# Optimization experiments

Hardware: AMD Instinct MI355X
Metric: run time of the kernel (lower is better)

## Reference

```python
import jax, jax.numpy as jnp
import numpy as np

B, S, H, T, NF = 64, 512, 1024, 4, 12
P = NF * (NF - 1) // 2  # 66 step pairs


def _head(x, w1, b1, w2, b2):
    # LinearsHead (eval mode: dropout = identity): linear -> relu -> linear
    return jax.nn.relu(x @ w1 + b1) @ w2 + b2


def setup_inputs() -> dict:
    key = jax.random.key(0)
    ks = jax.random.split(key, 12)
    sc = 0.02
    # non-overlapping contiguous spans: targets then facts, each L tokens
    L = S // (T + NF)  # 32
    t_start = jnp.arange(T, dtype=jnp.int32) * L
    f_start = (T + jnp.arange(NF, dtype=jnp.int32)) * L
    target_offsets = jnp.broadcast_to(jnp.stack([t_start, t_start + L], -1), (B, T, 2))
    fact_offsets = jnp.broadcast_to(jnp.stack([f_start, f_start + L], -1), (B, NF, 2))
    return {
        'seq_features': jax.random.normal(ks[0], (B, S, H), jnp.float32),
        'cls_features': jax.random.normal(ks[1], (B, H), jnp.float32),
        'target_offsets': target_offsets,
        'fact_offsets': fact_offsets,
        'fact_score_mask': jnp.ones((B, NF, T), jnp.float32),
        'sentsim_w1': sc * jax.random.normal(ks[2], (2 * H, H), jnp.float32),
        'sentsim_b1': jnp.zeros((H,), jnp.float32),
        'sentsim_w2': sc * jax.random.normal(ks[3], (H, 1), jnp.float32),
        'sentsim_b2': jnp.zeros((1,), jnp.float32),
        'step_w1': sc * jax.random.normal(ks[4], (2 * H, H), jnp.float32),
        'step_b1': jnp.zeros((H,), jnp.float32),
        'step_w2': sc * jax.random.normal(ks[5], (H, 1), jnp.float32),
        'step_b2': jnp.zeros((1,), jnp.float32),
        'state_w1': sc * jax.random.normal(ks[6], (H, H), jnp.float32),
        'state_b1': jnp.zeros((H,), jnp.float32),
        'state_w2': sc * jax.random.normal(ks[7], (H, 1), jnp.float32),
        'state_b2': jnp.zeros((1,), jnp.float32),
        'abd_w1': sc * jax.random.normal(ks[8], (2 * H, H), jnp.float32),
        'abd_b1': jnp.zeros((H,), jnp.float32),
        'abd_w2': sc * jax.random.normal(ks[9], (H, 1), jnp.float32),
        'abd_b2': jnp.zeros((1,), jnp.float32),
        'lambda_weight': jnp.array([0.5, 0.5], jnp.float32),
    }


def reference(seq_features, cls_features, target_offsets, fact_offsets, fact_score_mask,
              sentsim_w1, sentsim_b1, sentsim_w2, sentsim_b2,
              step_w1, step_b1, step_w2, step_b2,
              state_w1, state_b1, state_w2, state_b2,
              abd_w1, abd_b1, abd_w2, abd_b2, lambda_weight):
    b, s, h = seq_features.shape
    t = target_offsets.shape[1]
    nf = fact_offsets.shape[1]
    pos = jnp.arange(s)

    def seg_mean(offs):  # offs [b,k,2] -> mean-pooled [b,k,h]
        m = ((pos >= offs[..., 0:1]) & (pos < offs[..., 1:2])).astype(seq_features.dtype)
        cnt = (offs[..., 1] - offs[..., 0]).astype(seq_features.dtype)[..., None]
        return jnp.einsum('bks,bsh->bkh', m, seq_features) / cnt

    tgt = seg_mean(target_offsets)  # [b,t,h]
    fct = seg_mean(fact_offsets)    # [b,nf,h]

    # fact-cls pairs ordered target-major: features[ti*nf+fi] = cat(fact, target)
    ff = jnp.broadcast_to(fct[:, None], (b, t, nf, h))
    tt = jnp.broadcast_to(tgt[:, :, None], (b, t, nf, h))
    pair = jnp.concatenate([ff, tt], -1).reshape(b, t * nf, 2 * h)
    fact_score = jax.nn.sigmoid(_head(pair, sentsim_w1, sentsim_b1, sentsim_w2, sentsim_b2)[..., 0])  # [b, t*nf]
    # original does .view(len(facts), len(targets)) on the flat t-major scores
    mat = fact_score.reshape(b, nf, t)
    max_per_fact = jnp.max(mat * fact_score_mask, axis=2)  # [b, nf]
    state_fact = jnp.mean(max_per_fact, axis=1)            # [b]
    state_cls = jax.nn.sigmoid(_head(cls_features, state_w1, state_b1, state_w2, state_b2)[..., 0])
    w = jax.nn.softmax(lambda_weight)
    state = w[0] * state_fact + w[1] * state_cls           # [b]

    # step pairs: combinations(range(nf), 2) == row-major triu indices
    i1, i2 = jnp.triu_indices(nf, k=1)
    step_feat = jnp.concatenate([fct[:, i1], fct[:, i2]], -1)  # [b,P,2h]
    step = _head(step_feat, step_w1, step_b1, step_w2, step_b2)[..., 0]  # [b,P]

    tside = jnp.mean(tgt, axis=1)  # sum/len over targets [b,h]
    abd_feat = jnp.concatenate([jnp.broadcast_to(tside[:, None], (b, nf, h)), fct], -1)
    abd = _head(abd_feat, abd_w1, abd_b1, abd_w2, abd_b2)[..., 0]  # [b,nf]

    # step_func == 'softmax_all': joint softmax over step + abd scores
    allsc = jax.nn.softmax(jnp.concatenate([step, abd], axis=1), axis=1)
    np_pairs = i1.shape[0]
    step, abd = allsc[:, :np_pairs], allsc[:, np_pairs:]

    # pack: [state | fact_score | step | step_abd]
    return jnp.concatenate([state[:, None], fact_score, step, abd], axis=1)
```

## Files before the change

### kernel.cpp

```cpp
#include <hip/hip_runtime.h>
#include <hip/hip_bf16.h>

#define B_    64
#define S_    512
#define H_    1024
#define HH_   (H_*H_)
#define T_    4
#define NF_   12
#define TNF_  48
#define NP_   66
#define OUTC_ 127

#define NSENT_ (B_*TNF_)
#define NSTEP_ (B_*NP_)
#define NABD_  (B_*NF_)
#define NCLS_  (B_)
#define NWAVES_ (NSENT_+NSTEP_+NABD_+NCLS_)

#define AROW_FCT   0
#define AROW_TGT   768
#define AROW_TSD   1024
#define AROW_CLS   1088
#define AROWS_     1152

#define GROW_FSENT 0
#define GROW_S1    768
#define GROW_S2    1536
#define GROW_AF    2304
#define GROW_TSENT 3072
#define GROW_AT    3328
#define GROW_CLS   3392
#define GROWS_     3456

typedef __bf16 bf16x8 __attribute__((ext_vector_type(8)));
typedef float  f32x4  __attribute__((ext_vector_type(4)));
typedef __attribute__((address_space(1))) const unsigned int gcu32;
typedef __attribute__((address_space(3))) unsigned int lu32;

__device__ __forceinline__ ushort f2bf(float x) {
    union { float f; unsigned u; } c; c.f = x;
    unsigned r = c.u + 0x7fffu + ((c.u >> 16) & 1u);
    return (ushort)(r >> 16);
}
__device__ __forceinline__ float bflo(unsigned u) {
    union { unsigned u; float f; } c; c.u = u << 16; return c.f;
}
__device__ __forceinline__ float bfhi(unsigned u) {
    union { unsigned u; float f; } c; c.u = u & 0xffff0000u; return c.f;
}

__global__ __launch_bounds__(256) void prep_kernel(
    const float* __restrict__ seq, const int* __restrict__ toffs,
    const int* __restrict__ foffs, const float* __restrict__ cls,
    const float* __restrict__ sw1, const float* __restrict__ pw1,
    const float* __restrict__ aw1, const float* __restrict__ cw1,
    float* __restrict__ tgt32, ushort* __restrict__ Abf,
    ushort* __restrict__ Wt)
{
    int blk = blockIdx.x;
    int tid = threadIdx.x;

    if (blk < 1024) {
        int b = blk >> 4;
        int k = blk & 15;
        int start, end, arow;
        float* dst32 = nullptr;
        if (k < T_) {
            start = toffs[(b*T_ + k)*2];
            end   = toffs[(b*T_ + k)*2 + 1];
            dst32 = tgt32 + (size_t)(b*T_ + k) * H_;
            arow  = AROW_TGT + b*T_ + k;
        } else {
            int f = k - T_;
            start = foffs[(b*NF_ + f)*2];
            end   = foffs[(b*NF_ + f)*2 + 1];
            arow  = AROW_FCT + b*NF_ + f;
        }
        int h0 = tid * 4;
        const float* base = seq + ((size_t)b * S_ + start) * H_ + h0;
        float4 s = make_float4(0.f, 0.f, 0.f, 0.f);
        int n = end - start;
        #pragma unroll 4
        for (int r = 0; r < n; ++r) {
            float4 v = *(const float4*)(base + (size_t)r * H_);
            s.x += v.x; s.y += v.y; s.z += v.z; s.w += v.w;
        }
        float inv = 1.f / (float)n;
        s.x *= inv; s.y *= inv; s.z *= inv; s.w *= inv;
        if (dst32) *(float4*)(dst32 + h0) = s;
        ushort4 q; q.x = f2bf(s.x); q.y = f2bf(s.y); q.z = f2bf(s.z); q.w = f2bf(s.w);
        *(ushort4*)(Abf + (size_t)arow * H_ + h0) = q;
    } else if (blk < 1088) {
        int b = blk - 1024;
        int h0 = tid * 4;
        float4 c = *(const float4*)(cls + (size_t)b * H_ + h0);
        ushort4 qc; qc.x = f2bf(c.x); qc.y = f2bf(c.y); qc.z = f2bf(c.z); qc.w = f2bf(c.w);
        *(ushort4*)(Abf + (size_t)(AROW_CLS + b) * H_ + h0) = qc;
    } else {
        __shared__ float Tt[32][33];
        int idx2 = blk - 1088;
        int z = idx2 >> 10;
        int rem = idx2 & 1023;
        int k0 = (rem >> 5) * 32;
        int n0 = (rem & 31) * 32;
        const float* src;
        switch (z) {
            case 0: src = sw1; break;
            case 1: src = pw1; break;
            case 2: src = pw1 + HH_; break;
            case 3: src = aw1 + HH_; break;
            case 4: src = sw1 + HH_; break;
            case 5: src = aw1; break;
            default: src = cw1; break;
        }
        int ty = tid >> 3, tx = tid & 7;
        float4 v = *(const float4*)(src + (size_t)(k0 + ty) * H_ + n0 + tx*4);
        Tt[ty][tx*4 + 0] = v.x; Tt[ty][tx*4 + 1] = v.y;
        Tt[ty][tx*4 + 2] = v.z; Tt[ty][tx*4 + 3] = v.w;
        __syncthreads();
        int nx = ty, kx = tx;
        ushort4 q;
        q.x = f2bf(Tt[kx*4 + 0][nx]); q.y = f2bf(Tt[kx*4 + 1][nx]);
        q.z = f2bf(Tt[kx*4 + 2][nx]); q.w = f2bf(Tt[kx*4 + 3][nx]);
        *(ushort4*)(Wt + (size_t)z * HH_ + (size_t)(n0 + nx) * H_ + k0 + kx*4) = q;
    }
}

__global__ __launch_bounds__(256) void tside_kernel(
    const float* __restrict__ tgt32, ushort* __restrict__ Abf)
{
    int b = blockIdx.x;
    int h0 = threadIdx.x * 4;
    float4 s = make_float4(0.f, 0.f, 0.f, 0.f);
    for (int t = 0; t < T_; ++t) {
        float4 v = *(const float4*)(tgt32 + (size_t)(b*T_ + t)*H_ + h0);
        s.x += v.x; s.y += v.y; s.z += v.z; s.w += v.w;
    }
    ushort4 q;
    q.x = f2bf(s.x*0.25f); q.y = f2bf(s.y*0.25f);
    q.z = f2bf(s.z*0.25f); q.w = f2bf(s.w*0.25f);
    *(ushort4*)(Abf + (size_t)(AROW_TSD + b) * H_ + h0) = q;
}

__global__ __launch_bounds__(256) void gemm_bf16_kernel(
    const ushort* __restrict__ Abf, const ushort* __restrict__ Wt,
    ushort* __restrict__ G)
{
    __shared__ __align__(16) ushort As[2][64*32];
    __shared__ __align__(16) ushort Bs[2][128*32];

    int bx = blockIdx.x;
    int arow_base, wsel, grow_base, mt;
    if (bx < 48)      { int j = bx / 12; mt = bx % 12; arow_base = AROW_FCT; wsel = j; grow_base = j * 768; }
    else if (bx < 52) { mt = bx - 48; arow_base = AROW_TGT; wsel = 4; grow_base = GROW_TSENT; }
    else if (bx == 52){ mt = 0; arow_base = AROW_TSD; wsel = 5; grow_base = GROW_AT; }
    else              { mt = 0; arow_base = AROW_CLS; wsel = 6; grow_base = GROW_CLS; }

    const int tid  = threadIdx.x;
    const int lane = tid & 63;
    const int w    = tid >> 6;
    const int wr   = w >> 1, wc = w & 1;
    const int m0   = mt * 64;
    const int n0   = blockIdx.y * 128;

    const int srow  = lane >> 2;
    const int scol8 = (lane & 3) * 8;
    const ushort* gA  = Abf + (size_t)(arow_base + m0 + w*16 + srow) * H_ + scol8;
    const ushort* gB0 = Wt + (size_t)wsel * HH_ + (size_t)(n0 + w*32 + srow) * H_ + scol8;
    const ushort* gB1 = gB0 + (size_t)16 * H_;

    f32x4 acc00 = {0,0,0,0}, acc01 = {0,0,0,0}, acc02 = {0,0,0,0}, acc03 = {0,0,0,0};
    f32x4 acc10 = {0,0,0,0}, acc11 = {0,0,0,0}, acc12 = {0,0,0,0}, acc13 = {0,0,0,0};

    const int frow = lane & 15;
    const int fk   = (lane >> 4) * 8;

    #define STAGE(buf, kk) do {                                                   \
        __builtin_amdgcn_global_load_lds((gcu32*)(gA  + (kk)), (lu32*)(As[buf] + w*512), 16, 0, 0);          \
        __builtin_amdgcn_global_load_lds((gcu32*)(gB0 + (kk)), (lu32*)(Bs[buf] + w*1024), 16, 0, 0);         \
        __builtin_amdgcn_global_load_lds((gcu32*)(gB1 + (kk)), (lu32*)(Bs[buf] + w*1024 + 512), 16, 0, 0);   \
    } while (0)

    STAGE(0, 0);
    __syncthreads();

    #pragma unroll 1
    for (int t = 0; t < 32; ++t) {
        const int cur = t & 1;
        if (t < 31) STAGE(cur ^ 1, (t + 1) * 32);

        const ushort* pa = As[cur] + (wr*32 + frow) * 32 + fk;
        const ushort* pb = Bs[cur] + (wc*64 + frow) * 32 + fk;
        bf16x8 a0 = *(const bf16x8*)pa;
        bf16x8 a1 = *(const bf16x8*)(pa + 512);
        bf16x8 b0 = *(const bf16x8*)pb;
        bf16x8 b1 = *(const bf16x8*)(pb + 512);
        bf16x8 b2 = *(const bf16x8*)(pb + 1024);
        bf16x8 b3 = *(const bf16x8*)(pb + 1536);

        acc00 = __builtin_amdgcn_mfma_f32_16x16x32_bf16(a0, b0, acc00, 0, 0, 0);
        acc01 = __builtin_amdgcn_mfma_f32_16x16x32_bf16(a0, b1, acc01, 0, 0, 0);
        acc02 = __builtin_amdgcn_mfma_f32_16x16x32_bf16(a0, b2, acc02, 0, 0, 0);
        acc03 = __builtin_amdgcn_mfma_f32_16x16x32_bf16(a0, b3, acc03, 0, 0, 0);
        acc10 = __builtin_amdgcn_mfma_f32_16x16x32_bf16(a1, b0, acc10, 0, 0, 0);
        acc11 = __builtin_amdgcn_mfma_f32_16x16x32_bf16(a1, b1, acc11, 0, 0, 0);
        acc12 = __builtin_amdgcn_mfma_f32_16x16x32_bf16(a1, b2, acc12, 0, 0, 0);
        acc13 = __builtin_amdgcn_mfma_f32_16x16x32_bf16(a1, b3, acc13, 0, 0, 0);

        if (t < 31) __syncthreads();
    }
    #undef STAGE

    const int r0 = (lane >> 4) * 4;
    const int c  = lane & 15;
    const size_t rowb = (size_t)(grow_base + m0 + wr*32);
    const size_t colb = (size_t)(n0 + wc*64);
    #pragma unroll
    for (int r = 0; r < 4; ++r) {
        size_t ra = (rowb + r0 + r) * H_ + colb;
        size_t rb = (rowb + 16 + r0 + r) * H_ + colb;
        G[ra + 0  + c] = f2bf(acc00[r]);
        G[ra + 16 + c] = f2bf(acc01[r]);
        G[ra + 32 + c] = f2bf(acc02[r]);
        G[ra + 48 + c] = f2bf(acc03[r]);
        G[rb + 0  + c] = f2bf(acc10[r]);
        G[rb + 16 + c] = f2bf(acc11[r]);
        G[rb + 32 + c] = f2bf(acc12[r]);
        G[rb + 48 + c] = f2bf(acc13[r]);
    }
}

__global__ __launch_bounds__(256) void combine_kernel(
    const ushort* __restrict__ G,
    const float* __restrict__ sb1, const float* __restrict__ sw2,
    const float* __restrict__ pb1, const float* __restrict__ pw2,
    const float* __restrict__ ab1, const float* __restrict__ aw2,
    const float* __restrict__ cb1, const float* __restrict__ cw2,
    float* __restrict__ ssent, float* __restrict__ sstep,
    float* __restrict__ sabd, float* __restrict__ scls)
{
    int wv = blockIdx.x * 4 + (threadIdx.x >> 6);
    int lane = threadIdx.x & 63;
    if (wv >= NWAVES_) return;

    const ushort *U, *V;
    const float *b1, *w2;
    float* outp;
    if (wv < NSENT_) {
        int b = wv / TNF_, q = wv % TNF_;
        int t = q / NF_, f = q % NF_;
        U = G + (size_t)(GROW_FSENT + b*NF_ + f) * H_;
        V = G + (size_t)(GROW_TSENT + b*T_ + t) * H_;
        b1 = sb1; w2 = sw2; outp = ssent + wv;
    } else if (wv < NSENT_ + NSTEP_) {
        int s = wv - NSENT_;
        int b = s / NP_, p = s % NP_;
        int i = 0, rem = p, cnt = NF_ - 1;
        while (rem >= cnt) { rem -= cnt; --cnt; ++i; }
        int j = i + 1 + rem;
        U = G + (size_t)(GROW_S1 + b*NF_ + i) * H_;
        V = G + (size_t)(GROW_S2 + b*NF_ + j) * H_;
        b1 = pb1; w2 = pw2; outp = sstep + s;
    } else if (wv < NSENT_ + NSTEP_ + NABD_) {
        int s = wv - NSENT_ - NSTEP_;
        int b = s / NF_, f = s % NF_;
        U = G + (size_t)(GROW_AT + b) * H_;
        V = G + (size_t)(GROW_AF + b*NF_ + f) * H_;
        b1 = ab1; w2 = aw2; outp = sabd + s;
    } else {
        int b = wv - NSENT_ - NSTEP_ - NABD_;
        U = G + (size_t)(GROW_CLS + b) * H_;
        V = nullptr;
        b1 = cb1; w2 = cw2; outp = scls + b;
    }

    float acc = 0.f;
    #pragma unroll
    for (int h = 0; h < 2; ++h) {
        int nb = h * 512 + lane * 8;
        uint4 uu = *(const uint4*)(U + nb);
        float us[8] = { bflo(uu.x), bfhi(uu.x), bflo(uu.y), bfhi(uu.y),
                        bflo(uu.z), bfhi(uu.z), bflo(uu.w), bfhi(uu.w) };
        if (V) {
            uint4 vv = *(const uint4*)(V + nb);
            us[0] += bflo(vv.x); us[1] += bfhi(vv.x);
            us[2] += bflo(vv.y); us[3] += bfhi(vv.y);
            us[4] += bflo(vv.z); us[5] += bfhi(vv.z);
            us[6] += bflo(vv.w); us[7] += bfhi(vv.w);
        }
        float4 bA = *(const float4*)(b1 + nb);
        float4 bB = *(const float4*)(b1 + nb + 4);
        float4 wA = *(const float4*)(w2 + nb);
        float4 wB = *(const float4*)(w2 + nb + 4);
        acc = fmaf(fmaxf(us[0] + bA.x, 0.f), wA.x, acc);
        acc = fmaf(fmaxf(us[1] + bA.y, 0.f), wA.y, acc);
        acc = fmaf(fmaxf(us[2] + bA.z, 0.f), wA.z, acc);
        acc = fmaf(fmaxf(us[3] + bA.w, 0.f), wA.w, acc);
        acc = fmaf(fmaxf(us[4] + bB.x, 0.f), wB.x, acc);
        acc = fmaf(fmaxf(us[5] + bB.y, 0.f), wB.y, acc);
        acc = fmaf(fmaxf(us[6] + bB.z, 0.f), wB.z, acc);
        acc = fmaf(fmaxf(us[7] + bB.w, 0.f), wB.w, acc);
    }
    #pragma unroll
    for (int msk = 1; msk < 64; msk <<= 1)
        acc += __shfl_xor(acc, msk);
    if (lane == 0) *outp = acc;
}

__global__ __launch_bounds__(128) void finalize_kernel(
    const float* __restrict__ s_sent, const float* __restrict__ s_step,
    const float* __restrict__ s_abd, const float* __restrict__ s_cls,
    const float* __restrict__ mask, const float* __restrict__ lam,
    const float* __restrict__ sent_b2, const float* __restrict__ step_b2,
    const float* __restrict__ state_b2, const float* __restrict__ abd_b2,
    float* __restrict__ out)
{
    int b = blockIdx.x;
    int tid = threadIdx.x;
    __shared__ float fs[TNF_];
    __shared__ float sc[NP_ + NF_];
    __shared__ float mpf[NF_];
    __shared__ float smax, ssum;

    if (tid < TNF_) {
        float v = 1.f / (1.f + expf(-(s_sent[b*TNF_ + tid] + sent_b2[0])));
        fs[tid] = v;
        out[(size_t)b*OUTC_ + 1 + tid] = v;
    }
    if (tid < NP_)
        sc[tid] = s_step[b*NP_ + tid] + step_b2[0];
    else if (tid < NP_ + NF_)
        sc[tid] = s_abd[b*NF_ + (tid - NP_)] + abd_b2[0];
    __syncthreads();

    if (tid < NF_) {
        float m = -1e30f;
        for (int j = 0; j < T_; ++j)
            m = fmaxf(m, fs[tid*T_ + j] * mask[((size_t)b*NF_ + tid)*T_ + j]);
        mpf[tid] = m;
    }
    __syncthreads();

    if (tid == 0) {
        float sf = 0.f;
        for (int i = 0; i < NF_; ++i) sf += mpf[i];
        sf *= (1.f / NF_);
        float scls2 = 1.f / (1.f + expf(-(s_cls[b] + state_b2[0])));
        float l0 = lam[0], l1 = lam[1];
        float mx = fmaxf(l0, l1);
        float e0 = expf(l0 - mx), e1 = expf(l1 - mx);
        float w0 = e0 / (e0 + e1);
        out[(size_t)b*OUTC_] = w0 * sf + (1.f - w0) * scls2;
        float m2 = -1e30f;
        for (int i = 0; i < NP_ + NF_; ++i) m2 = fmaxf(m2, sc[i]);
        smax = m2;
    }
    __syncthreads();
    if (tid < NP_ + NF_) sc[tid] = expf(sc[tid] - smax);
    __syncthreads();
    if (tid == 0) {
        float s2 = 0.f;
        for (int i = 0; i < NP_ + NF_; ++i) s2 += sc[i];
        ssum = s2;
    }
    __syncthreads();
    if (tid < NP_ + NF_)
        out[(size_t)b*OUTC_ + 1 + TNF_ + tid] = sc[tid] / ssum;
}

extern "C" void kernel_launch(void* const* d_in, const int* in_sizes, int n_in,
                              void* d_out, int out_size, void* d_ws, size_t ws_size,
                              hipStream_t stream)
{
    (void)in_sizes; (void)n_in; (void)out_size; (void)ws_size;
    const float* seq  = (const float*)d_in[0];
    const float* cls  = (const float*)d_in[1];
    const int*   toff = (const int*)d_in[2];
    const int*   foff = (const int*)d_in[3];
    const float* mask = (const float*)d_in[4];
    const float* sw1  = (const float*)d_in[5];
    const float* sb1  = (const float*)d_in[6];
    const float* sw2  = (const float*)d_in[7];
    const float* sb2  = (const float*)d_in[8];
    const float* pw1  = (const float*)d_in[9];
    const float* pb1  = (const float*)d_in[10];
    const float* pw2  = (const float*)d_in[11];
    const float* pb2  = (const float*)d_in[12];
    const float* cw1  = (const float*)d_in[13];
    const float* cb1  = (const float*)d_in[14];
    const float* cw2  = (const float*)d_in[15];
    const float* cb2  = (const float*)d_in[16];
    const float* aw1  = (const float*)d_in[17];
    const float* ab1  = (const float*)d_in[18];
    const float* aw2  = (const float*)d_in[19];
    const float* ab2  = (const float*)d_in[20];
    const float* lam  = (const float*)d_in[21];

    char* wsb = (char*)d_ws;
    float*  tgt32 = (float*)wsb;
    float*  ssent = (float*)(wsb + (1u<<20));
    float*  sstep = ssent + NSENT_;
    float*  sabd  = sstep + NSTEP_;
    float*  scls  = sabd + NABD_;
    ushort* Abf   = (ushort*)(wsb + (1u<<20) + 32768);
    ushort* Wt    = Abf + (size_t)AROWS_ * H_;
    ushort* G     = Wt + (size_t)7 * HH_;

    prep_kernel<<<1088 + 7*1024, 256, 0, stream>>>(
        seq, toff, foff, cls, sw1, pw1, aw1, cw1, tgt32, Abf, Wt);

    tside_kernel<<<B_, 256, 0, stream>>>(tgt32, Abf);

    gemm_bf16_kernel<<<dim3(54, 8), 256, 0, stream>>>(Abf, Wt, G);

    combine_kernel<<<(NWAVES_ + 3) / 4, 256, 0, stream>>>(
        G, sb1, sw2, pb1, pw2, ab1, aw2, cb1, cw2,
        ssent, sstep, sabd, scls);

    finalize_kernel<<<B_, 128, 0, stream>>>(
        ssent, sstep, sabd, scls, mask, lam, sb2, pb2, cb2, ab2, (float*)d_out);
}
```

Before: 65.25 us.

## Enlarge GEMM tiles to 128x128 with swizzled LDS and deeper prefetch

The bf16 MFMA GEMM moves from 64x128 to 128x128 block tiles, so each wave computes a 4x4 grid of 16x16 accumulators and the grid shrinks from 54x8 to 28x8 blocks. LDS rows get an XOR swizzle on the k-chunk to cut bank conflicts. Loads are issued two stages ahead, using explicit vmcnt/lgkmcnt waits and raw barriers instead of __syncthreads. The A buffer is padded to 1280 rows so the half-used 64-row TSD and CLS tiles can read past their end, and stores are masked. The risks are fewer blocks than CUs on a 256-CU part and higher register pressure.

```diff
diff --git a/kernel.cpp b/kernel.cpp
--- a/kernel.cpp
+++ b/kernel.cpp
@@ -21,7 +21,7 @@
 #define AROW_TGT   768
 #define AROW_TSD   1024
 #define AROW_CLS   1088
-#define AROWS_     1152
+#define AROWS_PAD_ 1280
 
 #define GROW_FSENT 0
 #define GROW_S1    768
@@ -146,87 +146,111 @@
     const ushort* __restrict__ Abf, const ushort* __restrict__ Wt,
     ushort* __restrict__ G)
 {
-    __shared__ __align__(16) ushort As[2][64*32];
+    __shared__ __align__(16) ushort As[2][128*32];
     __shared__ __align__(16) ushort Bs[2][128*32];
 
     int bx = blockIdx.x;
-    int arow_base, wsel, grow_base, mt;
-    if (bx < 48)      { int j = bx / 12; mt = bx % 12; arow_base = AROW_FCT; wsel = j; grow_base = j * 768; }
-    else if (bx < 52) { mt = bx - 48; arow_base = AROW_TGT; wsel = 4; grow_base = GROW_TSENT; }
-    else if (bx == 52){ mt = 0; arow_base = AROW_TSD; wsel = 5; grow_base = GROW_AT; }
-    else              { mt = 0; arow_base = AROW_CLS; wsel = 6; grow_base = GROW_CLS; }
+    int arow_base, wsel, grow_base, m0, vrows;
+    if (bx < 24)      { int j = bx / 6; int mt = bx % 6; arow_base = AROW_FCT;
+                        wsel = j; grow_base = j * 768; m0 = mt * 128; vrows = 128; }
+    else if (bx < 26) { arow_base = AROW_TGT; wsel = 4; grow_base = GROW_TSENT;
+                        m0 = (bx - 24) * 128; vrows = 128; }
+    else if (bx == 26){ arow_base = AROW_TSD; wsel = 5; grow_base = GROW_AT;
+                        m0 = 0; vrows = 64; }
+    else              { arow_base = AROW_CLS; wsel = 6; grow_base = GROW_CLS;
+                        m0 = 0; vrows = 64; }
 
     const int tid  = threadIdx.x;
     const int lane = tid & 63;
     const int w    = tid >> 6;
     const int wr   = w >> 1, wc = w & 1;
-    const int m0   = mt * 64;
     const int n0   = blockIdx.y * 128;
 
-    const int srow  = lane >> 2;
-    const int scol8 = (lane & 3) * 8;
-    const ushort* gA  = Abf + (size_t)(arow_base + m0 + w*16 + srow) * H_ + scol8;
-    const ushort* gB0 = Wt + (size_t)wsel * HH_ + (size_t)(n0 + w*32 + srow) * H_ + scol8;
-    const ushort* gB1 = gB0 + (size_t)16 * H_;
-
-    f32x4 acc00 = {0,0,0,0}, acc01 = {0,0,0,0}, acc02 = {0,0,0,0}, acc03 = {0,0,0,0};
-    f32x4 acc10 = {0,0,0,0}, acc11 = {0,0,0,0}, acc12 = {0,0,0,0}, acc13 = {0,0,0,0};
-
-    const int frow = lane & 15;
-    const int fk   = (lane >> 4) * 8;
-
-    #define STAGE(buf, kk) do {                                                   \
-        __builtin_amdgcn_global_load_lds((gcu32*)(gA  + (kk)), (lu32*)(As[buf] + w*512), 16, 0, 0);          \
-        __builtin_amdgcn_global_load_lds((gcu32*)(gB0 + (kk)), (lu32*)(Bs[buf] + w*1024), 16, 0, 0);         \
-        __builtin_amdgcn_global_load_lds((gcu32*)(gB1 + (kk)), (lu32*)(Bs[buf] + w*1024 + 512), 16, 0, 0);   \
+    const int srow = lane >> 2;
+    const int scol = ((lane & 3) ^ ((lane >> 3) & 3)) * 8;
+    const ushort* gA0 = Abf + (size_t)(arow_base + m0 + w*16 + srow) * H_ + scol;
+    const ushort* gA1 = gA0 + (size_t)64 * H_;
+    const ushort* gB0 = Wt + (size_t)wsel * HH_
+                        + (size_t)(n0 + w*16 + srow) * H_ + scol;
+    const ushort* gB1 = gB0 + (size_t)64 * H_;
+    const int ldsA0 = (0*64 + w*16) * 32, ldsA1 = (1*64 + w*16) * 32;
+
+    const int frr  = lane & 15;
+    const int c0   = lane >> 4;
+    const int swz  = (frr >> 1) & 3;
+    const int offA = (wr*64 + frr) * 32 + (c0 ^ swz) * 8;
+    const int offB = (wc*64 + frr) * 32 + (c0 ^ swz) * 8;
+
+    f32x4 acc[4][4];
+    #pragma unroll
+    for (int i = 0; i < 4; ++i)
+        #pragma unroll
+        for (int j = 0; j < 4; ++j)
+            acc[i][j] = (f32x4){0.f, 0.f, 0.f, 0.f};
+
+    #define STAGE(buf, kstep) do {                                              \
+        int kk_ = (kstep) < 32 ? (kstep) * 32 : 0;                              \
+        __builtin_amdgcn_global_load_lds((gcu32*)(gA0 + kk_),                   \
+            (lu32*)(As[buf] + ldsA0), 16, 0, 0);                                \
+        __builtin_amdgcn_global_load_lds((gcu32*)(gA1 + kk_),                   \
+            (lu32*)(As[buf] + ldsA1), 16, 0, 0);                                \
+        __builtin_amdgcn_global_load_lds((gcu32*)(gB0 + kk_),                   \
+            (lu32*)(Bs[buf] + ldsA0), 16, 0, 0);                                \
+        __builtin_amdgcn_global_load_lds((gcu32*)(gB1 + kk_),                   \
+            (lu32*)(Bs[buf] + ldsA1), 16, 0, 0);                                \
     } while (0)
 
     STAGE(0, 0);
-    __syncthreads();
+    STAGE(1, 1);
 
     #pragma unroll 1
     for (int t = 0; t < 32; ++t) {
         const int cur = t & 1;
-        if (t < 31) STAGE(cur ^ 1, (t + 1) * 32);
-
-        const ushort* pa = As[cur] + (wr*32 + frow) * 32 + fk;
-        const ushort* pb = Bs[cur] + (wc*64 + frow) * 32 + fk;
-        bf16x8 a0 = *(const bf16x8*)pa;
-        bf16x8 a1 = *(const bf16x8*)(pa + 512);
-        bf16x8 b0 = *(const bf16x8*)pb;
-        bf16x8 b1 = *(const bf16x8*)(pb + 512);
-        bf16x8 b2 = *(const bf16x8*)(pb + 1024);
-        bf16x8 b3 = *(const bf16x8*)(pb + 1536);
-
-        acc00 = __builtin_amdgcn_mfma_f32_16x16x32_bf16(a0, b0, acc00, 0, 0, 0);
-        acc01 = __builtin_amdgcn_mfma_f32_16x16x32_bf16(a0, b1, acc01, 0, 0, 0);
-        acc02 = __builtin_amdgcn_mfma_f32_16x16x32_bf16(a0, b2, acc02, 0, 0, 0);
-        acc03 = __builtin_amdgcn_mfma_f32_16x16x32_bf16(a0, b3, acc03, 0, 0, 0);
-        acc10 = __builtin_amdgcn_mfma_f32_16x16x32_bf16(a1, b0, acc10, 0, 0, 0);
-        acc11 = __builtin_amdgcn_mfma_f32_16x16x32_bf16(a1, b1, acc11, 0, 0, 0);
-        acc12 = __builtin_amdgcn_mfma_f32_16x16x32_bf16(a1, b2, acc12, 0, 0, 0);
-        acc13 = __builtin_amdgcn_mfma_f32_16x16x32_bf16(a1, b3, acc13, 0, 0, 0);
-
-        if (t < 31) __syncthreads();
+        asm volatile("s_waitcnt vmcnt(4)" ::: "memory");
+        __builtin_amdgcn_s_barrier();
+        __builtin_amdgcn_sched_barrier(0);
+
+        const ushort* pa = As[cur] + offA;
+        const ushort* pb = Bs[cur] + offB;
+        bf16x8 a0 = *(const bf16x8*)(pa);
+        bf16x8 a1 = *(const bf16x8*)(pa + 16*32);
+        bf16x8 a2 = *(const bf16x8*)(pa + 32*32);
+        bf16x8 a3 = *(const bf16x8*)(pa + 48*32);
+        bf16x8 b0 = *(const bf16x8*)(pb);
+        bf16x8 b1 = *(const bf16x8*)(pb + 16*32);
+        bf16x8 b2 = *(const bf16x8*)(pb + 32*32);
+        bf16x8 b3 = *(const bf16x8*)(pb + 48*32);
+
+        asm volatile("s_waitcnt lgkmcnt(0)" ::: "memory");
+        __builtin_amdgcn_s_barrier();
+        __builtin_amdgcn_sched_barrier(0);
+
+        if (t < 30) STAGE(cur, t + 2);
+
+        bf16x8 av[4] = {a0, a1, a2, a3};
+        bf16x8 bv[4] = {b0, b1, b2, b3};
+        #pragma unroll
+        for (int i = 0; i < 4; ++i)
+            #pragma unroll
+            for (int j = 0; j < 4; ++j)
+                acc[i][j] = __builtin_amdgcn_mfma_f32_16x16x32_bf16(
+                    av[i], bv[j], acc[i][j], 0, 0, 0);
     }
     #undef STAGE
 
     const int r0 = (lane >> 4) * 4;
-    const int c  = lane & 15;
-    const size_t rowb = (size_t)(grow_base + m0 + wr*32);
-    const size_t colb = (size_t)(n0 + wc*64);
+    const int cc = lane & 15;
     #pragma unroll
-    for (int r = 0; r < 4; ++r) {
-        size_t ra = (rowb + r0 + r) * H_ + colb;
-        size_t rb = (rowb + 16 + r0 + r) * H_ + colb;
-        G[ra + 0  + c] = f2bf(acc00[r]);
-        G[ra + 16 + c] = f2bf(acc01[r]);
-        G[ra + 32 + c] = f2bf(acc02[r]);
-        G[ra + 48 + c] = f2bf(acc03[r]);
-        G[rb + 0  + c] = f2bf(acc10[r]);
-        G[rb + 16 + c] = f2bf(acc11[r]);
-        G[rb + 32 + c] = f2bf(acc12[r]);
-        G[rb + 48 + c] = f2bf(acc13[r]);
+    for (int i = 0; i < 4; ++i) {
+        int lrow = wr*64 + i*16 + r0;
+        if (lrow >= vrows) continue;
+        #pragma unroll
+        for (int r = 0; r < 4; ++r) {
+            size_t gr = (size_t)(grow_base + m0 + lrow + r) * H_ + n0 + wc*64 + cc;
+            #pragma unroll
+            for (int j = 0; j < 4; ++j)
+                G[gr + j*16] = f2bf(acc[i][j][r]);
+        }
     }
 }
 
@@ -403,7 +427,7 @@
     float*  sabd  = sstep + NSTEP_;
     float*  scls  = sabd + NABD_;
     ushort* Abf   = (ushort*)(wsb + (1u<<20) + 32768);
-    ushort* Wt    = Abf + (size_t)AROWS_ * H_;
+    ushort* Wt    = Abf + (size_t)AROWS_PAD_ * H_;
     ushort* G     = Wt + (size_t)7 * HH_;
 
     prep_kernel<<<1088 + 7*1024, 256, 0, stream>>>(
@@ -411,7 +435,7 @@
 
     tside_kernel<<<B_, 256, 0, stream>>>(tgt32, Abf);
 
-    gemm_bf16_kernel<<<dim3(54, 8), 256, 0, stream>>>(Abf, Wt, G);
+    gemm_bf16_kernel<<<dim3(28, 8), 256, 0, stream>>>(Abf, Wt, G);
 
     combine_kernel<<<(NWAVES_ + 3) / 4, 256, 0, stream>>>(
         G, sb1, sw2, pb1, pw2, ab1, aw2, cb1, cw2,
```

After: 62.45 us. 1.04x faster.

## Shrink GEMM tiles to 64x64 with two waves and swizzle LDS layout

Applied to the files above, without the earlier changes.

The bf16 GEMM tile shrinks from 64x128 with four waves to 64x64 with two waves, and the grid doubles along N to 54x16 blocks so more blocks are resident across CUs. Double buffering is dropped in favour of single-buffered LDS with two barriers per k-step. An XOR swizzle is added to the LDS row layout to reduce bank conflicts on the fragment reads. The aim is more parallelism for a small GEMM, at the cost of less load/compute overlap and more re-reads of A from global memory.

```diff
diff --git a/kernel.cpp b/kernel.cpp
--- a/kernel.cpp
+++ b/kernel.cpp
@@ -142,91 +142,89 @@
     *(ushort4*)(Abf + (size_t)(AROW_TSD + b) * H_ + h0) = q;
 }
 
-__global__ __launch_bounds__(256) void gemm_bf16_kernel(
+__global__ __launch_bounds__(128) void gemm_bf16_kernel(
     const ushort* __restrict__ Abf, const ushort* __restrict__ Wt,
     ushort* __restrict__ G)
 {
-    __shared__ __align__(16) ushort As[2][64*32];
-    __shared__ __align__(16) ushort Bs[2][128*32];
-
-    int bx = blockIdx.x;
-    int arow_base, wsel, grow_base, mt;
-    if (bx < 48)      { int j = bx / 12; mt = bx % 12; arow_base = AROW_FCT; wsel = j; grow_base = j * 768; }
-    else if (bx < 52) { mt = bx - 48; arow_base = AROW_TGT; wsel = 4; grow_base = GROW_TSENT; }
-    else if (bx == 52){ mt = 0; arow_base = AROW_TSD; wsel = 5; grow_base = GROW_AT; }
-    else              { mt = 0; arow_base = AROW_CLS; wsel = 6; grow_base = GROW_CLS; }
+    __shared__ __align__(16) ushort As[64*32];
+    __shared__ __align__(16) ushort Bs[64*32];
+
+    const int mt = blockIdx.x;
+    const int n0 = blockIdx.y * 64;
+
+    int arow, wsel, grow;
+    if (mt < 48)      { wsel = mt / 12; int m = mt % 12;
+                        arow = AROW_FCT + m*64; grow = wsel*768 + m*64; }
+    else if (mt < 52) { wsel = 4; arow = AROW_TGT + (mt-48)*64;
+                        grow = GROW_TSENT + (mt-48)*64; }
+    else if (mt == 52){ wsel = 5; arow = AROW_TSD; grow = GROW_AT; }
+    else              { wsel = 6; arow = AROW_CLS; grow = GROW_CLS; }
 
     const int tid  = threadIdx.x;
     const int lane = tid & 63;
     const int w    = tid >> 6;
-    const int wr   = w >> 1, wc = w & 1;
-    const int m0   = mt * 64;
-    const int n0   = blockIdx.y * 128;
-
-    const int srow  = lane >> 2;
-    const int scol8 = (lane & 3) * 8;
-    const ushort* gA  = Abf + (size_t)(arow_base + m0 + w*16 + srow) * H_ + scol8;
-    const ushort* gB0 = Wt + (size_t)wsel * HH_ + (size_t)(n0 + w*32 + srow) * H_ + scol8;
+
+    const int srow = lane >> 2;
+    const int scol = ((lane & 3) ^ ((lane >> 3) & 3)) * 8;
+    const ushort* gA0 = Abf + (size_t)(arow + w*32 + srow) * H_ + scol;
+    const ushort* gA1 = gA0 + (size_t)16 * H_;
+    const ushort* gB0 = Wt + (size_t)wsel * HH_
+                        + (size_t)(n0 + w*32 + srow) * H_ + scol;
     const ushort* gB1 = gB0 + (size_t)16 * H_;
-
-    f32x4 acc00 = {0,0,0,0}, acc01 = {0,0,0,0}, acc02 = {0,0,0,0}, acc03 = {0,0,0,0};
-    f32x4 acc10 = {0,0,0,0}, acc11 = {0,0,0,0}, acc12 = {0,0,0,0}, acc13 = {0,0,0,0};
-
-    const int frow = lane & 15;
-    const int fk   = (lane >> 4) * 8;
-
-    #define STAGE(buf, kk) do {                                                   \
-        __builtin_amdgcn_global_load_lds((gcu32*)(gA  + (kk)), (lu32*)(As[buf] + w*512), 16, 0, 0);          \
-        __builtin_amdgcn_global_load_lds((gcu32*)(gB0 + (kk)), (lu32*)(Bs[buf] + w*1024), 16, 0, 0);         \
-        __builtin_amdgcn_global_load_lds((gcu32*)(gB1 + (kk)), (lu32*)(Bs[buf] + w*1024 + 512), 16, 0, 0);   \
-    } while (0)
-
-    STAGE(0, 0);
-    __syncthreads();
+    ushort* ldsA = As + w * 1024;
+    ushort* ldsB = Bs + w * 1024;
+
+    const int frr  = lane & 15;
+    const int c0   = lane >> 4;
+    const int swz8 = (c0 ^ ((frr >> 1) & 3)) * 8;
+    const int offA = (w*32 + frr) * 32 + swz8;
+    const int offB = frr * 32 + swz8;
+
+    f32x4 acc[2][4];
+    #pragma unroll
+    for (int i = 0; i < 2; ++i)
+        #pragma unroll
+        for (int j = 0; j < 4; ++j)
+            acc[i][j] = (f32x4){0.f, 0.f, 0.f, 0.f};
 
     #pragma unroll 1
     for (int t = 0; t < 32; ++t) {
-        const int cur = t & 1;
-        if (t < 31) STAGE(cur ^ 1, (t + 1) * 32);
-
-        const ushort* pa = As[cur] + (wr*32 + frow) * 32 + fk;
-        const ushort* pb = Bs[cur] + (wc*64 + frow) * 32 + fk;
-        bf16x8 a0 = *(const bf16x8*)pa;
-        bf16x8 a1 = *(const bf16x8*)(pa + 512);
-        bf16x8 b0 = *(const bf16x8*)pb;
-        bf16x8 b1 = *(const bf16x8*)(pb + 512);
-        bf16x8 b2 = *(const bf16x8*)(pb + 1024);
-        bf16x8 b3 = *(const bf16x8*)(pb + 1536);
-
-        acc00 = __builtin_amdgcn_mfma_f32_16x16x32_bf16(a0, b0, acc00, 0, 0, 0);
-        acc01 = __builtin_amdgcn_mfma_f32_16x16x32_bf16(a0, b1, acc01, 0, 0, 0);
-        acc02 = __builtin_amdgcn_mfma_f32_16x16x32_bf16(a0, b2, acc02, 0, 0, 0);
-        acc03 = __builtin_amdgcn_mfma_f32_16x16x32_bf16(a0, b3, acc03, 0, 0, 0);
-        acc10 = __builtin_amdgcn_mfma_f32_16x16x32_bf16(a1, b0, acc10, 0, 0, 0);
-        acc11 = __builtin_amdgcn_mfma_f32_16x16x32_bf16(a1, b1, acc11, 0, 0, 0);
-        acc12 = __builtin_amdgcn_mfma_f32_16x16x32_bf16(a1, b2, acc12, 0, 0, 0);
-        acc13 = __builtin_amdgcn_mfma_f32_16x16x32_bf16(a1, b3, acc13, 0, 0, 0);
-
-        if (t < 31) __syncthreads();
-    }
-    #undef STAGE
+        const int kk = t * 32;
+        __syncthreads();
+        __builtin_amdgcn_global_load_lds((gcu32*)(gA0 + kk), (lu32*)ldsA,         16, 0, 0);
+        __builtin_amdgcn_global_load_lds((gcu32*)(gA1 + kk), (lu32*)(ldsA + 512), 16, 0, 0);
+        __builtin_amdgcn_global_load_lds((gcu32*)(gB0 + kk), (lu32*)ldsB,         16, 0, 0);
+        __builtin_amdgcn_global_load_lds((gcu32*)(gB1 + kk), (lu32*)(ldsB + 512), 16, 0, 0);
+        __syncthreads();
+
+        bf16x8 a0 = *(const bf16x8*)(As + offA);
+        bf16x8 a1 = *(const bf16x8*)(As + offA + 512);
+        bf16x8 b0 = *(const bf16x8*)(Bs + offB);
+        bf16x8 b1 = *(const bf16x8*)(Bs + offB + 512);
+        bf16x8 b2 = *(const bf16x8*)(Bs + offB + 1024);
+        bf16x8 b3 = *(const bf16x8*)(Bs + offB + 1536);
+
+        acc[0][0] = __builtin_amdgcn_mfma_f32_16x16x32_bf16(a0, b0, acc[0][0], 0, 0, 0);
+        acc[0][1] = __builtin_amdgcn_mfma_f32_16x16x32_bf16(a0, b1, acc[0][1], 0, 0, 0);
+        acc[0][2] = __builtin_amdgcn_mfma_f32_16x16x32_bf16(a0, b2, acc[0][2], 0, 0, 0);
+        acc[0][3] = __builtin_amdgcn_mfma_f32_16x16x32_bf16(a0, b3, acc[0][3], 0, 0, 0);
+        acc[1][0] = __builtin_amdgcn_mfma_f32_16x16x32_bf16(a1, b0, acc[1][0], 0, 0, 0);
+        acc[1][1] = __builtin_amdgcn_mfma_f32_16x16x32_bf16(a1, b1, acc[1][1], 0, 0, 0);
+        acc[1][2] = __builtin_amdgcn_mfma_f32_16x16x32_bf16(a1, b2, acc[1][2], 0, 0, 0);
+        acc[1][3] = __builtin_amdgcn_mfma_f32_16x16x32_bf16(a1, b3, acc[1][3], 0, 0, 0);
+    }
 
     const int r0 = (lane >> 4) * 4;
-    const int c  = lane & 15;
-    const size_t rowb = (size_t)(grow_base + m0 + wr*32);
-    const size_t colb = (size_t)(n0 + wc*64);
+    const int cc = lane & 15;
     #pragma unroll
-    for (int r = 0; r < 4; ++r) {
-        size_t ra = (rowb + r0 + r) * H_ + colb;
-        size_t rb = (rowb + 16 + r0 + r) * H_ + colb;
-        G[ra + 0  + c] = f2bf(acc00[r]);
-        G[ra + 16 + c] = f2bf(acc01[r]);
-        G[ra + 32 + c] = f2bf(acc02[r]);
-        G[ra + 48 + c] = f2bf(acc03[r]);
-        G[rb + 0  + c] = f2bf(acc10[r]);
-        G[rb + 16 + c] = f2bf(acc11[r]);
-        G[rb + 32 + c] = f2bf(acc12[r]);
-        G[rb + 48 + c] = f2bf(acc13[r]);
+    for (int i = 0; i < 2; ++i) {
+        #pragma unroll
+        for (int r = 0; r < 4; ++r) {
+            size_t gr = (size_t)(grow + w*32 + i*16 + r0 + r) * H_ + n0 + cc;
+            #pragma unroll
+            for (int j = 0; j < 4; ++j)
+                G[gr + j*16] = f2bf(acc[i][j][r]);
+        }
     }
 }
 
@@ -411,7 +409,7 @@
 
     tside_kernel<<<B_, 256, 0, stream>>>(tgt32, Abf);
 
-    gemm_bf16_kernel<<<dim3(54, 8), 256, 0, stream>>>(Abf, Wt, G);
+    gemm_bf16_kernel<<<dim3(54, 16), 128, 0, stream>>>(Abf, Wt, G);
 
     combine_kernel<<<(NWAVES_ + 3) / 4, 256, 0, stream>>>(
         G, sb1, sw2, pb1, pw2, ab1, aw2, cb1, cw2,
```

Measured after the change: 65.07 us. Within noise of the previous version (-0.3%).
